# Kernel tuning notes

Hardware: AMD Instinct MI355X
Metric: run time of the kernel (lower is better)

Reference implementation:

```python
import jax, jax.numpy as jnp
import numpy as np

B, C, N = 8, 512, 2048  # batch, channels (=size), tokens


def setup_inputs() -> dict:
    key = jax.random.key(0)
    ks = jax.random.split(key, 9)
    s = 1.0 / np.sqrt(C)
    return {
        "q": jax.random.normal(ks[0], (B, C, N), dtype=jnp.float32),
        "k": jax.random.normal(ks[1], (B, C, N), dtype=jnp.float32),
        "v": jax.random.normal(ks[2], (B, C, N), dtype=jnp.float32),
        "wq": jax.random.normal(ks[3], (C, C), dtype=jnp.float32) * s,
        "bq": jax.random.normal(ks[4], (C,), dtype=jnp.float32) * s,
        "wk": jax.random.normal(ks[5], (C, C), dtype=jnp.float32) * s,
        "bk": jax.random.normal(ks[6], (C,), dtype=jnp.float32) * s,
        "wv": jax.random.normal(ks[7], (C, C), dtype=jnp.float32) * s,
        "bv": jax.random.normal(ks[8], (C,), dtype=jnp.float32) * s,
    }


def _proj(x, w, b):
    # 1x1 conv over channels: out[b,c,n] = sum_i w[c,i] x[b,i,n] + b[c]
    return jnp.einsum('ci,bin->bcn', w, x) + b[None, :, None]


def reference(q, k, v, wq, bq, wk, bk, wv, bv):
    residual = q                                   # [B, C, N]
    qp = _proj(q, wq, bq).transpose(0, 2, 1)       # [B, N, C]
    kp = _proj(k, wk, bk).transpose(0, 2, 1)       # [B, N, C]
    vp = _proj(v, wv, bv).transpose(0, 2, 1)       # [B, N, C]
    attn = jnp.einsum('bnc,bmc->bnm', qp, kp)      # raw QK^T, no scale/softmax
    out = jnp.einsum('bnm,bmc->bnc', attn, vp)     # [B, N, C]
    return out.transpose(0, 2, 1) + residual       # [B, C, N]
```

## Files before the change

### kernel.cpp

```cpp
#include <hip/hip_runtime.h>
#include <hip/hip_bf16.h>
#include <stdint.h>

#define B_ 8
#define C_ 512
#define N_ 2048

typedef __bf16 bf16_t;
typedef bf16_t bf16x8 __attribute__((ext_vector_type(8)));
typedef bf16_t bf16x4 __attribute__((ext_vector_type(4)));
typedef float f32x4 __attribute__((ext_vector_type(4)));

__global__ __launch_bounds__(256) void weights_kernel(
    const float* __restrict__ wq, const float* __restrict__ wk,
    const float* __restrict__ wv, const float* __restrict__ bq,
    const float* __restrict__ bk,
    bf16_t* __restrict__ WqT, bf16_t* __restrict__ WkT,
    bf16_t* __restrict__ Wvb, float* __restrict__ s1p)
{
    __shared__ bf16_t tile[64][65];
    __shared__ float red[256];
    const int t = blockIdx.x;
    const int tid = threadIdx.x;
    if (t < 128) {
        const float* src = (t < 64) ? wq : wk;
        bf16_t* dst = (t < 64) ? WqT : WkT;
        const int j = t & 63;
        const int i0 = (j & 7) * 64, c0 = (j >> 3) * 64;
        const int cx = (tid & 15) * 4, ry = tid >> 4;
#pragma unroll
        for (int r = ry; r < 64; r += 16) {
            float4 f = *(const float4*)&src[(size_t)(c0 + r) * C_ + i0 + cx];
            tile[r][cx + 0] = (bf16_t)f.x; tile[r][cx + 1] = (bf16_t)f.y;
            tile[r][cx + 2] = (bf16_t)f.z; tile[r][cx + 3] = (bf16_t)f.w;
        }
        __syncthreads();
#pragma unroll
        for (int r = ry; r < 64; r += 16) {
            bf16x4 o;
            o[0] = tile[cx + 0][r]; o[1] = tile[cx + 1][r];
            o[2] = tile[cx + 2][r]; o[3] = tile[cx + 3][r];
            *(bf16x4*)&dst[(size_t)(i0 + r) * C_ + c0 + cx] = o;
        }
    } else if (t < 192) {
        const int j = t - 128;
#pragma unroll
        for (int p = 0; p < 4; ++p) {
            const int i = j * 4096 + p * 1024 + tid * 4;
            float4 f = *(const float4*)(wv + i);
            bf16x4 o;
            o[0] = (bf16_t)f.x; o[1] = (bf16_t)f.y;
            o[2] = (bf16_t)f.z; o[3] = (bf16_t)f.w;
            *(bf16x4*)(Wvb + i) = o;
        }
    } else {
        float p = bk[tid] * bq[tid] + bk[tid + 256] * bq[tid + 256];
        red[tid] = p;
        __syncthreads();
        for (int s = 128; s > 0; s >>= 1) {
            if (tid < s) red[tid] += red[tid + s];
            __syncthreads();
        }
        if (tid == 0) s1p[0] = red[0];
    }
}

__global__ __launch_bounds__(256) void gemm_M_aux(
    const bf16_t* __restrict__ WqT, const bf16_t* __restrict__ WkT,
    bf16_t* __restrict__ M, const float* __restrict__ bq,
    const float* __restrict__ bk, float* __restrict__ gk,
    float* __restrict__ va)
{
    __shared__ __align__(16) bf16_t As[64 * 64];
    __shared__ __align__(16) bf16_t Bs[64 * 64];
    const int tid = threadIdx.x;
    if (blockIdx.x < 64) {
        const int lane = tid & 63, wave = tid >> 6;
        const int wr = wave >> 1, wc = wave & 1;
        const int m0 = (blockIdx.x >> 3) * 64, n0 = (blockIdx.x & 7) * 64;
        const int K = C_;
        f32x4 acc[2][2];
#pragma unroll
        for (int i = 0; i < 2; ++i)
#pragma unroll
            for (int j = 0; j < 2; ++j) acc[i][j] = 0.f;
        const int srow = tid >> 3;
        const int scol = ((tid & 7) ^ (srow & 7)) * 8;
        const int ldso = tid * 16;
        for (int t = 0; t < 8; ++t) {
            const bf16_t* ga = WqT + (size_t)(m0 + srow) * K + t * 64 + scol;
            const bf16_t* gb = WkT + (size_t)(n0 + srow) * K + t * 64 + scol;
#pragma unroll
            for (int p = 0; p < 2; ++p)
                __builtin_amdgcn_global_load_lds(
                    (const __attribute__((address_space(1))) void*)(ga + (size_t)p * 32 * K),
                    (__attribute__((address_space(3))) void*)((char*)As + ldso + p * 4096),
                    16, 0, 0);
#pragma unroll
            for (int p = 0; p < 2; ++p)
                __builtin_amdgcn_global_load_lds(
                    (const __attribute__((address_space(1))) void*)(gb + (size_t)p * 32 * K),
                    (__attribute__((address_space(3))) void*)((char*)Bs + ldso + p * 4096),
                    16, 0, 0);
            __syncthreads();
#pragma unroll
            for (int kk = 0; kk < 64; kk += 32) {
                bf16x8 af[2], bfr[2];
                const int kcol = kk + (lane >> 4) * 8;
                const int kc = kcol >> 3;
#pragma unroll
                for (int m = 0; m < 2; ++m) {
                    const int r = wr * 32 + (lane & 15) + m * 16;
                    af[m] = *(const bf16x8*)((const char*)As + r * 128 +
                                             ((kc ^ (r & 7)) << 4));
                }
#pragma unroll
                for (int n = 0; n < 2; ++n) {
                    const int r = wc * 32 + (lane & 15) + n * 16;
                    bfr[n] = *(const bf16x8*)((const char*)Bs + r * 128 +
                                              ((kc ^ (r & 7)) << 4));
                }
#pragma unroll
                for (int m = 0; m < 2; ++m)
#pragma unroll
                    for (int n = 0; n < 2; ++n)
                        acc[m][n] = __builtin_amdgcn_mfma_f32_16x16x32_bf16(
                            af[m], bfr[n], acc[m][n], 0, 0, 0);
            }
            __syncthreads();
        }
        const int rj = (lane >> 4) * 4;
        const int cc = lane & 15;
#pragma unroll
        for (int m = 0; m < 2; ++m)
#pragma unroll
            for (int n = 0; n < 2; ++n) {
                const int col = n0 + wc * 32 + n * 16 + cc;
                f32x4 vv = acc[m][n];
#pragma unroll
                for (int j = 0; j < 4; ++j) {
                    const int row = m0 + wr * 32 + m * 16 + rj + j;
                    M[(size_t)row * C_ + col] = (bf16_t)vv[j];
                }
            }
    } else {
        const int j = (int)blockIdx.x - 64;
        const bf16_t* W = (j < 8) ? WkT : WqT;
        const float* bb = (j < 8) ? bq : bk;
        float* out = (j < 8) ? gk : va;
        const int row = (j & 7) * 64 + (tid >> 2);
        const int c0 = (tid & 3) * 128;
        const bf16_t* rp = W + (size_t)row * C_ + c0;
        float acc = 0.f;
#pragma unroll
        for (int e = 0; e < 128; e += 8) {
            bf16x8 vv = *(const bf16x8*)(rp + e);
#pragma unroll
            for (int x = 0; x < 8; ++x) acc += (float)vv[x] * bb[c0 + e + x];
        }
        acc += __shfl_xor(acc, 1, 64);
        acc += __shfl_xor(acc, 2, 64);
        if ((tid & 3) == 0) out[row] = acc;
    }
}

__global__ __launch_bounds__(256) void prep_kernel(
    const float* __restrict__ kin, const float* __restrict__ vin,
    const float* __restrict__ q,
    bf16_t* __restrict__ kc, bf16_t* __restrict__ vc,
    bf16_t* __restrict__ qT, bf16_t* __restrict__ qc,
    float* __restrict__ sk, float* __restrict__ sv)
{
    __shared__ bf16_t tile[64][65];
    __shared__ float red[4];
    const int bid = blockIdx.x;
    const int tid = threadIdx.x;
    if (bid < 8192) {
        const int row = bid & 4095;
        const int selv = bid >> 12;
        const float* src = (selv ? vin : kin) + (size_t)row * N_;
        bf16_t* dst = (selv ? vc : kc) + (size_t)row * N_;
        const int i = tid * 8;
        float4 f0 = *(const float4*)(src + i);
        float4 f1 = *(const float4*)(src + i + 4);
        bf16x8 o;
        o[0] = (bf16_t)f0.x; o[1] = (bf16_t)f0.y; o[2] = (bf16_t)f0.z; o[3] = (bf16_t)f0.w;
        o[4] = (bf16_t)f1.x; o[5] = (bf16_t)f1.y; o[6] = (bf16_t)f1.z; o[7] = (bf16_t)f1.w;
        *(bf16x8*)(dst + i) = o;
        float s = f0.x + f0.y + f0.z + f0.w + f1.x + f1.y + f1.z + f1.w;
#pragma unroll
        for (int d = 1; d < 64; d <<= 1) s += __shfl_xor(s, d, 64);
        if ((tid & 63) == 0) red[tid >> 6] = s;
        __syncthreads();
        if (tid == 0)
            (selv ? sv : sk)[row] = red[0] + red[1] + red[2] + red[3];
    } else {
        const int t = bid - 8192;
        const int b = t >> 8;
        const int rem = t & 255;
        const int c0 = (rem >> 5) * 64;
        const int n0 = (rem & 31) * 64;
        const float* src = q + (size_t)b * C_ * N_;
        bf16_t* dT = qT + (size_t)b * N_ * C_;
        bf16_t* dc = qc + (size_t)b * C_ * N_;
        const int cx = (tid & 15) * 4, ry = tid >> 4;
#pragma unroll
        for (int r = ry; r < 64; r += 16) {
            float4 f = *(const float4*)&src[(size_t)(c0 + r) * N_ + n0 + cx];
            bf16x4 o;
            o[0] = (bf16_t)f.x; o[1] = (bf16_t)f.y;
            o[2] = (bf16_t)f.z; o[3] = (bf16_t)f.w;
            tile[r][cx + 0] = o[0]; tile[r][cx + 1] = o[1];
            tile[r][cx + 2] = o[2]; tile[r][cx + 3] = o[3];
            *(bf16x4*)&dc[(size_t)(c0 + r) * N_ + n0 + cx] = o;
        }
        __syncthreads();
#pragma unroll
        for (int r = ry; r < 64; r += 16) {
            bf16x4 o;
            o[0] = tile[cx + 0][r]; o[1] = tile[cx + 1][r];
            o[2] = tile[cx + 2][r]; o[3] = tile[cx + 3][r];
            *(bf16x4*)&dT[(size_t)(n0 + r) * C_ + c0 + cx] = o;
        }
    }
}

template <int SPLITS>
__global__ __launch_bounds__(256, 2) void gemm_ntK(
    const bf16_t* __restrict__ A, const bf16_t* __restrict__ Bm,
    bf16_t* __restrict__ Cout,
    int Nn, int K, size_t sA, size_t sB, size_t sC)
{
    __shared__ __align__(16) bf16_t As[128 * 64];
    __shared__ __align__(16) bf16_t Bs[128 * 64];

    const int tid = threadIdx.x, lane = tid & 63, wave = tid >> 6;
    const int wr = wave >> 1, wc = wave & 1;
    const int bz = blockIdx.z / SPLITS;
    const int sp = blockIdx.z % SPLITS;
    const int kbeg = sp * (K / SPLITS);
    const int nt = (K / SPLITS) / 64;

    const bf16_t* Ab = A + (size_t)bz * sA;
    const bf16_t* Bb = Bm + (size_t)bz * sB;
    const int m0 = blockIdx.y * 128, n0 = blockIdx.x * 128;

    f32x4 acc[4][4];
#pragma unroll
    for (int i = 0; i < 4; ++i)
#pragma unroll
        for (int j = 0; j < 4; ++j) acc[i][j] = 0.f;

    const int srow = tid >> 3;
    const int scol = ((tid & 7) ^ (srow & 7)) * 8;
    const int ldso = tid * 16;

    for (int t = 0; t < nt; ++t) {
        const bf16_t* ga = Ab + (size_t)(m0 + srow) * K + kbeg + t * 64 + scol;
        const bf16_t* gb = Bb + (size_t)(n0 + srow) * K + kbeg + t * 64 + scol;
#pragma unroll
        for (int p = 0; p < 4; ++p)
            __builtin_amdgcn_global_load_lds(
                (const __attribute__((address_space(1))) void*)(ga + (size_t)p * 32 * K),
                (__attribute__((address_space(3))) void*)((char*)As + ldso + p * 4096),
                16, 0, 0);
#pragma unroll
        for (int p = 0; p < 4; ++p)
            __builtin_amdgcn_global_load_lds(
                (const __attribute__((address_space(1))) void*)(gb + (size_t)p * 32 * K),
                (__attribute__((address_space(3))) void*)((char*)Bs + ldso + p * 4096),
                16, 0, 0);
        __syncthreads();

#pragma unroll
        for (int kk = 0; kk < 64; kk += 32) {
            bf16x8 af[4], bfr[4];
            const int kcol = kk + (lane >> 4) * 8;
            const int kc = kcol >> 3;
#pragma unroll
            for (int m = 0; m < 4; ++m) {
                const int r = wr * 64 + (lane & 15) + m * 16;
                af[m] = *(const bf16x8*)((const char*)As + r * 128 +
                                         ((kc ^ (r & 7)) << 4));
            }
#pragma unroll
            for (int n = 0; n < 4; ++n) {
                const int r = wc * 64 + (lane & 15) + n * 16;
                bfr[n] = *(const bf16x8*)((const char*)Bs + r * 128 +
                                          ((kc ^ (r & 7)) << 4));
            }
#pragma unroll
            for (int m = 0; m < 4; ++m)
#pragma unroll
                for (int n = 0; n < 4; ++n)
                    acc[m][n] = __builtin_amdgcn_mfma_f32_16x16x32_bf16(
                        af[m], bfr[n], acc[m][n], 0, 0, 0);
        }
        __syncthreads();
    }

    const int rj = (lane >> 4) * 4;
    const int cc = lane & 15;
#pragma unroll
    for (int m = 0; m < 4; ++m) {
#pragma unroll
        for (int n = 0; n < 4; ++n) {
            const int col = n0 + wc * 64 + n * 16 + cc;
            f32x4 vv = acc[m][n];
#pragma unroll
            for (int j = 0; j < 4; ++j) {
                const int row = m0 + wr * 64 + m * 16 + rj + j;
                Cout[(size_t)blockIdx.z * sC + (size_t)row * Nn + col] = (bf16_t)vv[j];
            }
        }
    }
}

__global__ __launch_bounds__(256) void reduce_mv_kernel(
    const bf16_t* __restrict__ Pt, bf16_t* __restrict__ Out,
    const bf16_t* __restrict__ Wvb, const bf16_t* __restrict__ M,
    const float* __restrict__ sk, const float* __restrict__ sv,
    const float* __restrict__ gk, const float* __restrict__ s1p,
    float* __restrict__ u, float* __restrict__ vbraw, float* __restrict__ s2)
{
    __shared__ float svec[C_];
    __shared__ float red[256];
    const size_t sCC = (size_t)C_ * C_;
    const int bid = blockIdx.x, tid = threadIdx.x;
    if (bid < 1024) {
        size_t idx = ((size_t)bid * 256 + tid) * 8;
        size_t b = idx / sCC;
        size_t r = idx - b * sCC;
        const bf16_t* base = Pt + (b * 4) * sCC + r;
        float acc[8];
#pragma unroll
        for (int j = 0; j < 8; ++j) acc[j] = 0.f;
#pragma unroll
        for (int s = 0; s < 4; ++s) {
            bf16x8 pv = *(const bf16x8*)(base + (size_t)s * sCC);
#pragma unroll
            for (int j = 0; j < 8; ++j) acc[j] += (float)pv[j];
        }
        bf16x8 o;
#pragma unroll
        for (int j = 0; j < 8; ++j) o[j] = (bf16_t)acc[j];
        *(bf16x8*)(Out + idx) = o;
    } else if (bid < 1032) {
        const int b = bid - 1024;
        const float* s4 = sv + (size_t)b * C_;
#pragma unroll
        for (int rr = 0; rr < 2; ++rr) {
            const int j = tid * 2 + rr;
            svec[j] = s4[j];
        }
        __syncthreads();
        const int c = tid * 2;
#pragma unroll
        for (int rr = 0; rr < 2; ++rr) {
            const bf16_t* row = Wvb + (size_t)(c + rr) * C_;
            float acc = 0.f;
            for (int j = 0; j < C_; j += 8) {
                bf16x8 vv = *(const bf16x8*)(row + j);
#pragma unroll
                for (int e = 0; e < 8; ++e) acc += (float)vv[e] * svec[j + e];
            }
            u[b * C_ + c + rr] = acc;
        }
    } else {
        const int b = bid - 1032;
        const float* s4 = sk + (size_t)b * C_;
#pragma unroll
        for (int rr = 0; rr < 2; ++rr) {
            const int j = tid * 2 + rr;
            svec[j] = s4[j];
        }
        __syncthreads();
        const int c = tid * 2;
#pragma unroll
        for (int rr = 0; rr < 2; ++rr) {
            const bf16_t* row = M + (size_t)(c + rr) * C_;
            float acc = 0.f;
            for (int j = 0; j < C_; j += 8) {
                bf16x8 vv = *(const bf16x8*)(row + j);
#pragma unroll
                for (int e = 0; e < 8; ++e) acc += (float)vv[e] * svec[j + e];
            }
            vbraw[b * C_ + c + rr] = acc;
        }
        float p = svec[tid] * gk[tid] + svec[tid + 256] * gk[tid + 256];
        red[tid] = p;
        __syncthreads();
        for (int s = 128; s > 0; s >>= 1) {
            if (tid < s) red[tid] += red[tid + s];
            __syncthreads();
        }
        if (tid == 0) s2[b] = red[0] + 2048.0f * s1p[0];
    }
}

template <int EPI>
__global__ __launch_bounds__(256) void gemm64_nt(
    const bf16_t* __restrict__ A, const bf16_t* __restrict__ Bm,
    bf16_t* __restrict__ Cout, size_t sA, size_t sB, size_t sC,
    const float* __restrict__ e0, const float* __restrict__ e1,
    const float* __restrict__ e2, const float* __restrict__ e3,
    const float* __restrict__ bqv, float* __restrict__ hout,
    const float* __restrict__ s1p, const float* __restrict__ s2p)
{
    __shared__ __align__(16) bf16_t As[64 * 64];
    __shared__ __align__(16) bf16_t Bs[64 * 64];

    const int tid = threadIdx.x, lane = tid & 63, wave = tid >> 6;
    const int wr = wave >> 1, wc = wave & 1;
    const int bz = blockIdx.z;
    const int m0 = blockIdx.y * 64, n0 = blockIdx.x * 64;
    const int K = C_;

    const bf16_t* Ab = A + (size_t)bz * sA;
    const bf16_t* Bb = Bm + (size_t)bz * sB;

    f32x4 acc[2][2];
#pragma unroll
    for (int i = 0; i < 2; ++i)
#pragma unroll
        for (int j = 0; j < 2; ++j) acc[i][j] = 0.f;

    const int srow = tid >> 3;
    const int scol = ((tid & 7) ^ (srow & 7)) * 8;
    const int ldso = tid * 16;

    float hacc = 0.f;
    const bool doH = (EPI == 3) && (blockIdx.x == 0);

    for (int t = 0; t < 8; ++t) {
        const bf16_t* ga = Ab + (size_t)(m0 + srow) * K + t * 64 + scol;
        const bf16_t* gb = Bb + (size_t)(n0 + srow) * K + t * 64 + scol;
#pragma unroll
        for (int p = 0; p < 2; ++p)
            __builtin_amdgcn_global_load_lds(
                (const __attribute__((address_space(1))) void*)(ga + (size_t)p * 32 * K),
                (__attribute__((address_space(3))) void*)((char*)As + ldso + p * 4096),
                16, 0, 0);
#pragma unroll
        for (int p = 0; p < 2; ++p)
            __builtin_amdgcn_global_load_lds(
                (const __attribute__((address_space(1))) void*)(gb + (size_t)p * 32 * K),
                (__attribute__((address_space(3))) void*)((char*)Bs + ldso + p * 4096),
                16, 0, 0);
        __syncthreads();

#pragma unroll
        for (int kk = 0; kk < 64; kk += 32) {
            bf16x8 af[2], bfr[2];
            const int kcol = kk + (lane >> 4) * 8;
            const int kc = kcol >> 3;
#pragma unroll
            for (int m = 0; m < 2; ++m) {
                const int r = wr * 32 + (lane & 15) + m * 16;
                af[m] = *(const bf16x8*)((const char*)As + r * 128 +
                                         ((kc ^ (r & 7)) << 4));
            }
#pragma unroll
            for (int n = 0; n < 2; ++n) {
                const int r = wc * 32 + (lane & 15) + n * 16;
                bfr[n] = *(const bf16x8*)((const char*)Bs + r * 128 +
                                          ((kc ^ (r & 7)) << 4));
            }
#pragma unroll
            for (int m = 0; m < 2; ++m)
#pragma unroll
                for (int n = 0; n < 2; ++n)
                    acc[m][n] = __builtin_amdgcn_mfma_f32_16x16x32_bf16(
                        af[m], bfr[n], acc[m][n], 0, 0, 0);
        }
        if (doH) {
            const int rr = tid >> 2, qq = tid & 3;
#pragma unroll
            for (int u = 0; u < 2; ++u) {
                const int c = qq * 2 + u;
                bf16x8 av = *(const bf16x8*)((const char*)As + rr * 128 +
                                             ((c ^ (rr & 7)) << 4));
                const float* bp = bqv + t * 64 + c * 8;
#pragma unroll
                for (int e = 0; e < 8; ++e) hacc += (float)av[e] * bp[e];
            }
        }
        __syncthreads();
    }

    const int rj = (lane >> 4) * 4;
    const int cc = lane & 15;
#pragma unroll
    for (int m = 0; m < 2; ++m) {
#pragma unroll
        for (int n = 0; n < 2; ++n) {
            const int col = n0 + wc * 32 + n * 16 + cc;
            f32x4 vv = acc[m][n];
#pragma unroll
            for (int j = 0; j < 4; ++j) {
                const int row = m0 + wr * 32 + m * 16 + rj + j;
                float val = vv[j];
                if (EPI == 3)
                    val += e0[bz * C_ + row] * e1[col] +
                           e2[row] * (e3[bz * C_ + col] + 2048.0f * e1[col]);
                Cout[(size_t)bz * sC + (size_t)row * C_ + col] = (bf16_t)val;
            }
        }
    }
    if (doH) {
        hacc += __shfl_xor(hacc, 1, 64);
        hacc += __shfl_xor(hacc, 2, 64);
        if ((tid & 3) == 0) {
            const int row = m0 + (tid >> 2);
            hout[bz * C_ + row] = hacc + e0[bz * C_ + row] * s1p[0] +
                                  e2[row] * s2p[bz];
        }
    }
}

__global__ __launch_bounds__(256) void gemm_final(
    const bf16_t* __restrict__ A, const bf16_t* __restrict__ Bm,
    float* __restrict__ Cout, const bf16_t* __restrict__ qc,
    const float* __restrict__ hvec)
{
    __shared__ __align__(16) bf16_t As[128 * 64];
    __shared__ __align__(16) bf16_t Bs[128 * 64];

    const int f = blockIdx.x;
    const int xcd = f & 7, sl = f >> 3;
    const int g = xcd + 8 * (sl >> 2);
    const int m0 = (sl & 3) * 128;
    const int bz = g >> 4;
    const int n0 = (g & 15) * 128;
    const int K = C_;

    const int tid = threadIdx.x, lane = tid & 63, wave = tid >> 6;
    const int wr = wave >> 1, wc = wave & 1;

    const bf16_t* Ab = A + (size_t)bz * ((size_t)C_ * C_);
    const bf16_t* Bb = Bm + (size_t)bz * ((size_t)N_ * C_);

    f32x4 acc[4][4];
#pragma unroll
    for (int i = 0; i < 4; ++i)
#pragma unroll
        for (int j = 0; j < 4; ++j) acc[i][j] = 0.f;

    const int srow = tid >> 3;
    const int scol = ((tid & 7) ^ (srow & 7)) * 8;
    const int ldso = tid * 16;

    for (int t = 0; t < 8; ++t) {
        const bf16_t* ga = Ab + (size_t)(m0 + srow) * K + t * 64 + scol;
        const bf16_t* gb = Bb + (size_t)(n0 + srow) * K + t * 64 + scol;
#pragma unroll
        for (int p = 0; p < 4; ++p)
            __builtin_amdgcn_global_load_lds(
                (const __attribute__((address_space(1))) void*)(ga + (size_t)p * 32 * K),
                (__attribute__((address_space(3))) void*)((char*)As + ldso + p * 4096),
                16, 0, 0);
#pragma unroll
        for (int p = 0; p < 4; ++p)
            __builtin_amdgcn_global_load_lds(
                (const __attribute__((address_space(1))) void*)(gb + (size_t)p * 32 * K),
                (__attribute__((address_space(3))) void*)((char*)Bs + ldso + p * 4096),
                16, 0, 0);
        __syncthreads();

#pragma unroll
        for (int kk = 0; kk < 64; kk += 32) {
            bf16x8 af[4], bfr[4];
            const int kcol = kk + (lane >> 4) * 8;
            const int kc = kcol >> 3;
#pragma unroll
            for (int m = 0; m < 4; ++m) {
                const int r = wr * 64 + (lane & 15) + m * 16;
                af[m] = *(const bf16x8*)((const char*)As + r * 128 +
                                         ((kc ^ (r & 7)) << 4));
            }
#pragma unroll
            for (int n = 0; n < 4; ++n) {
                const int r = wc * 64 + (lane & 15) + n * 16;
                bfr[n] = *(const bf16x8*)((const char*)Bs + r * 128 +
                                          ((kc ^ (r & 7)) << 4));
            }
#pragma unroll
            for (int m = 0; m < 4; ++m)
#pragma unroll
                for (int n = 0; n < 4; ++n)
                    acc[m][n] = __builtin_amdgcn_mfma_f32_16x16x32_bf16(
                        af[m], bfr[n], acc[m][n], 0, 0, 0);
        }
        __syncthreads();
    }

    const int rj = (lane >> 4) * 4;
    const int cc = lane & 15;
    const size_t ob = (size_t)bz * ((size_t)C_ * N_);
#pragma unroll
    for (int m = 0; m < 4; ++m) {
#pragma unroll
        for (int n = 0; n < 4; ++n) {
            const int col = n0 + wc * 64 + n * 16 + cc;
            f32x4 vv = acc[m][n];
#pragma unroll
            for (int j = 0; j < 4; ++j) {
                const int row = m0 + wr * 64 + m * 16 + rj + j;
                const size_t o = ob + (size_t)row * N_ + col;
                Cout[o] = vv[j] + hvec[bz * C_ + row] + (float)qc[o];
            }
        }
    }
}

extern "C" void kernel_launch(void* const* d_in, const int* in_sizes, int n_in,
                              void* d_out, int out_size, void* d_ws, size_t ws_size,
                              hipStream_t stream)
{
    (void)in_sizes; (void)n_in; (void)out_size; (void)ws_size;
    const float* q  = (const float*)d_in[0];
    const float* k  = (const float*)d_in[1];
    const float* v  = (const float*)d_in[2];
    const float* wq = (const float*)d_in[3];
    const float* bq = (const float*)d_in[4];
    const float* wk = (const float*)d_in[5];
    const float* bk = (const float*)d_in[6];
    const float* wv = (const float*)d_in[7];
    const float* bv = (const float*)d_in[8];
    float* out = (float*)d_out;

    char* ws = (char*)d_ws;
    const size_t WSZ = (size_t)C_ * C_ * 2;
    const size_t TSZ = (size_t)B_ * N_ * C_ * 2;
    const size_t SCZ = (size_t)B_ * C_ * C_ * 2;
    const size_t VSZ = (size_t)B_ * C_ * 4;
    const size_t sCC = (size_t)C_ * C_;
    const size_t sBN = (size_t)N_ * C_;
    size_t off = 0;
    bf16_t* WqTb = (bf16_t*)(ws + off); off += WSZ;
    bf16_t* WkTb = (bf16_t*)(ws + off); off += WSZ;
    bf16_t* Wvb  = (bf16_t*)(ws + off); off += WSZ;
    bf16_t* M    = (bf16_t*)(ws + off); off += WSZ;
    bf16_t* qT   = (bf16_t*)(ws + off); off += TSZ;
    bf16_t* qc   = (bf16_t*)(ws + off); off += TSZ;
    bf16_t* kc   = (bf16_t*)(ws + off); off += TSZ;
    bf16_t* vc   = (bf16_t*)(ws + off); off += TSZ;
    bf16_t* Dp   = (bf16_t*)(ws + off); off += TSZ;
    bf16_t* D    = (bf16_t*)(ws + off); off += SCZ;
    bf16_t* P1   = (bf16_t*)(ws + off); off += SCZ;
    bf16_t* HT   = (bf16_t*)(ws + off); off += SCZ;
    float*  sk   = (float*)(ws + off);  off += VSZ;
    float*  sv   = (float*)(ws + off);  off += VSZ;
    float*  gk   = (float*)(ws + off);  off += C_ * 4;
    float*  va   = (float*)(ws + off);  off += C_ * 4;
    float*  s1p  = (float*)(ws + off);  off += 64;
    float*  s2   = (float*)(ws + off);  off += 64;
    float*  uu   = (float*)(ws + off);  off += VSZ;
    float*  vbr  = (float*)(ws + off);  off += VSZ;
    float*  hb   = (float*)(ws + off);  off += VSZ;

    const dim3 blk(256);

    weights_kernel<<<dim3(193), blk, 0, stream>>>(
        wq, wk, wv, bq, bk, WqTb, WkTb, Wvb, s1p);

    gemm_M_aux<<<dim3(80), blk, 0, stream>>>(WqTb, WkTb, M, bq, bk, gk, va);

    prep_kernel<<<dim3(10240), blk, 0, stream>>>(
        k, v, q, kc, vc, qT, qc, sk, sv);

    gemm_ntK<4><<<dim3(C_ / 128, C_ / 128, B_ * 4), blk, 0, stream>>>(
        kc, vc, Dp, C_, N_, sBN, sBN, sCC);

    reduce_mv_kernel<<<dim3(1040), blk, 0, stream>>>(
        Dp, D, Wvb, M, sk, sv, gk, s1p, uu, vbr, s2);

    gemm64_nt<0><<<dim3(8, 8, B_), blk, 0, stream>>>(
        Wvb, D, P1, 0, sCC, sCC,
        nullptr, nullptr, nullptr, nullptr, nullptr, nullptr, nullptr, nullptr);

    gemm64_nt<3><<<dim3(8, 8, B_), blk, 0, stream>>>(
        P1, M, HT, sCC, 0, sCC, uu, va, bv, vbr, gk, hb, s1p, s2);

    gemm_final<<<dim3(512), blk, 0, stream>>>(HT, qT, out, qc, hb);
}
```

Before: 118.7 us.

## Fuse prep, weight and GEMM stages into fewer kernel launches

Merges the weight-conversion kernel into the input-prep kernel, moves the M=WqT·WkT GEMM and bias matvecs into the same launch as the split-K K·V^T GEMM, and fuses the split-K reduction with the Wv·D GEMM into one kernel. It also drops the bf16 copy of q and reads the fp32 residual directly in the final GEMM epilogue. The aim is to cut launch count from eight to five and remove one bf16 write/read pass over q, at the cost of heterogeneous blocks within each launch and a different residual precision path.

```diff
diff --git a/kernel.cpp b/kernel.cpp
--- a/kernel.cpp
+++ b/kernel.cpp
@@ -11,26 +11,33 @@
 typedef bf16_t bf16x4 __attribute__((ext_vector_type(4)));
 typedef float f32x4 __attribute__((ext_vector_type(4)));
 
-__global__ __launch_bounds__(256) void weights_kernel(
+__global__ __launch_bounds__(256) void prep_all_kernel(
+    const float* __restrict__ q, const float* __restrict__ kin,
+    const float* __restrict__ vin,
     const float* __restrict__ wq, const float* __restrict__ wk,
     const float* __restrict__ wv, const float* __restrict__ bq,
     const float* __restrict__ bk,
-    bf16_t* __restrict__ WqT, bf16_t* __restrict__ WkT,
-    bf16_t* __restrict__ Wvb, float* __restrict__ s1p)
+    bf16_t* __restrict__ qT, bf16_t* __restrict__ kc, bf16_t* __restrict__ vc,
+    bf16_t* __restrict__ WqT, bf16_t* __restrict__ WkT, bf16_t* __restrict__ Wvb,
+    float* __restrict__ s1p, float* __restrict__ sk, float* __restrict__ sv)
 {
     __shared__ bf16_t tile[64][65];
-    __shared__ float red[256];
-    const int t = blockIdx.x;
+    __shared__ float red256[256];
+    __shared__ float red4[4];
+    const int bid = blockIdx.x;
     const int tid = threadIdx.x;
-    if (t < 128) {
-        const float* src = (t < 64) ? wq : wk;
-        bf16_t* dst = (t < 64) ? WqT : WkT;
-        const int j = t & 63;
-        const int i0 = (j & 7) * 64, c0 = (j >> 3) * 64;
+
+    if (bid < 2048) {
+        const int b = bid >> 8;
+        const int rem = bid & 255;
+        const int c0 = (rem >> 5) * 64;
+        const int n0 = (rem & 31) * 64;
+        const float* src = q + (size_t)b * C_ * N_;
+        bf16_t* dT = qT + (size_t)b * N_ * C_;
         const int cx = (tid & 15) * 4, ry = tid >> 4;
 #pragma unroll
         for (int r = ry; r < 64; r += 16) {
-            float4 f = *(const float4*)&src[(size_t)(c0 + r) * C_ + i0 + cx];
+            float4 f = *(const float4*)&src[(size_t)(c0 + r) * N_ + n0 + cx];
             tile[r][cx + 0] = (bf16_t)f.x; tile[r][cx + 1] = (bf16_t)f.y;
             tile[r][cx + 2] = (bf16_t)f.z; tile[r][cx + 3] = (bf16_t)f.w;
         }
@@ -40,144 +47,55 @@
             bf16x4 o;
             o[0] = tile[cx + 0][r]; o[1] = tile[cx + 1][r];
             o[2] = tile[cx + 2][r]; o[3] = tile[cx + 3][r];
-            *(bf16x4*)&dst[(size_t)(i0 + r) * C_ + c0 + cx] = o;
-        }
-    } else if (t < 192) {
-        const int j = t - 128;
-#pragma unroll
-        for (int p = 0; p < 4; ++p) {
-            const int i = j * 4096 + p * 1024 + tid * 4;
-            float4 f = *(const float4*)(wv + i);
-            bf16x4 o;
-            o[0] = (bf16_t)f.x; o[1] = (bf16_t)f.y;
-            o[2] = (bf16_t)f.z; o[3] = (bf16_t)f.w;
-            *(bf16x4*)(Wvb + i) = o;
+            *(bf16x4*)&dT[(size_t)(n0 + r) * C_ + c0 + cx] = o;
+        }
+    } else if (bid < 2241) {
+        const int t = bid - 2048;
+        if (t < 128) {
+            const float* src = (t < 64) ? wq : wk;
+            bf16_t* dst = (t < 64) ? WqT : WkT;
+            const int j = t & 63;
+            const int i0 = (j & 7) * 64, c0 = (j >> 3) * 64;
+            const int cx = (tid & 15) * 4, ry = tid >> 4;
+#pragma unroll
+            for (int r = ry; r < 64; r += 16) {
+                float4 f = *(const float4*)&src[(size_t)(c0 + r) * C_ + i0 + cx];
+                tile[r][cx + 0] = (bf16_t)f.x; tile[r][cx + 1] = (bf16_t)f.y;
+                tile[r][cx + 2] = (bf16_t)f.z; tile[r][cx + 3] = (bf16_t)f.w;
+            }
+            __syncthreads();
+#pragma unroll
+            for (int r = ry; r < 64; r += 16) {
+                bf16x4 o;
+                o[0] = tile[cx + 0][r]; o[1] = tile[cx + 1][r];
+                o[2] = tile[cx + 2][r]; o[3] = tile[cx + 3][r];
+                *(bf16x4*)&dst[(size_t)(i0 + r) * C_ + c0 + cx] = o;
+            }
+        } else if (t < 192) {
+            const int j = t - 128;
+#pragma unroll
+            for (int p = 0; p < 4; ++p) {
+                const int i = j * 4096 + p * 1024 + tid * 4;
+                float4 f = *(const float4*)(wv + i);
+                bf16x4 o;
+                o[0] = (bf16_t)f.x; o[1] = (bf16_t)f.y;
+                o[2] = (bf16_t)f.z; o[3] = (bf16_t)f.w;
+                *(bf16x4*)(Wvb + i) = o;
+            }
+        } else {
+            float p = bk[tid] * bq[tid] + bk[tid + 256] * bq[tid + 256];
+            red256[tid] = p;
+            __syncthreads();
+            for (int s = 128; s > 0; s >>= 1) {
+                if (tid < s) red256[tid] += red256[tid + s];
+                __syncthreads();
+            }
+            if (tid == 0) s1p[0] = red256[0];
         }
     } else {
-        float p = bk[tid] * bq[tid] + bk[tid + 256] * bq[tid + 256];
-        red[tid] = p;
-        __syncthreads();
-        for (int s = 128; s > 0; s >>= 1) {
-            if (tid < s) red[tid] += red[tid + s];
-            __syncthreads();
-        }
-        if (tid == 0) s1p[0] = red[0];
-    }
-}
-
-__global__ __launch_bounds__(256) void gemm_M_aux(
-    const bf16_t* __restrict__ WqT, const bf16_t* __restrict__ WkT,
-    bf16_t* __restrict__ M, const float* __restrict__ bq,
-    const float* __restrict__ bk, float* __restrict__ gk,
-    float* __restrict__ va)
-{
-    __shared__ __align__(16) bf16_t As[64 * 64];
-    __shared__ __align__(16) bf16_t Bs[64 * 64];
-    const int tid = threadIdx.x;
-    if (blockIdx.x < 64) {
-        const int lane = tid & 63, wave = tid >> 6;
-        const int wr = wave >> 1, wc = wave & 1;
-        const int m0 = (blockIdx.x >> 3) * 64, n0 = (blockIdx.x & 7) * 64;
-        const int K = C_;
-        f32x4 acc[2][2];
-#pragma unroll
-        for (int i = 0; i < 2; ++i)
-#pragma unroll
-            for (int j = 0; j < 2; ++j) acc[i][j] = 0.f;
-        const int srow = tid >> 3;
-        const int scol = ((tid & 7) ^ (srow & 7)) * 8;
-        const int ldso = tid * 16;
-        for (int t = 0; t < 8; ++t) {
-            const bf16_t* ga = WqT + (size_t)(m0 + srow) * K + t * 64 + scol;
-            const bf16_t* gb = WkT + (size_t)(n0 + srow) * K + t * 64 + scol;
-#pragma unroll
-            for (int p = 0; p < 2; ++p)
-                __builtin_amdgcn_global_load_lds(
-                    (const __attribute__((address_space(1))) void*)(ga + (size_t)p * 32 * K),
-                    (__attribute__((address_space(3))) void*)((char*)As + ldso + p * 4096),
-                    16, 0, 0);
-#pragma unroll
-            for (int p = 0; p < 2; ++p)
-                __builtin_amdgcn_global_load_lds(
-                    (const __attribute__((address_space(1))) void*)(gb + (size_t)p * 32 * K),
-                    (__attribute__((address_space(3))) void*)((char*)Bs + ldso + p * 4096),
-                    16, 0, 0);
-            __syncthreads();
-#pragma unroll
-            for (int kk = 0; kk < 64; kk += 32) {
-                bf16x8 af[2], bfr[2];
-                const int kcol = kk + (lane >> 4) * 8;
-                const int kc = kcol >> 3;
-#pragma unroll
-                for (int m = 0; m < 2; ++m) {
-                    const int r = wr * 32 + (lane & 15) + m * 16;
-                    af[m] = *(const bf16x8*)((const char*)As + r * 128 +
-                                             ((kc ^ (r & 7)) << 4));
-                }
-#pragma unroll
-                for (int n = 0; n < 2; ++n) {
-                    const int r = wc * 32 + (lane & 15) + n * 16;
-                    bfr[n] = *(const bf16x8*)((const char*)Bs + r * 128 +
-                                              ((kc ^ (r & 7)) << 4));
-                }
-#pragma unroll
-                for (int m = 0; m < 2; ++m)
-#pragma unroll
-                    for (int n = 0; n < 2; ++n)
-                        acc[m][n] = __builtin_amdgcn_mfma_f32_16x16x32_bf16(
-                            af[m], bfr[n], acc[m][n], 0, 0, 0);
-            }
-            __syncthreads();
-        }
-        const int rj = (lane >> 4) * 4;
-        const int cc = lane & 15;
-#pragma unroll
-        for (int m = 0; m < 2; ++m)
-#pragma unroll
-            for (int n = 0; n < 2; ++n) {
-                const int col = n0 + wc * 32 + n * 16 + cc;
-                f32x4 vv = acc[m][n];
-#pragma unroll
-                for (int j = 0; j < 4; ++j) {
-                    const int row = m0 + wr * 32 + m * 16 + rj + j;
-                    M[(size_t)row * C_ + col] = (bf16_t)vv[j];
-                }
-            }
-    } else {
-        const int j = (int)blockIdx.x - 64;
-        const bf16_t* W = (j < 8) ? WkT : WqT;
-        const float* bb = (j < 8) ? bq : bk;
-        float* out = (j < 8) ? gk : va;
-        const int row = (j & 7) * 64 + (tid >> 2);
-        const int c0 = (tid & 3) * 128;
-        const bf16_t* rp = W + (size_t)row * C_ + c0;
-        float acc = 0.f;
-#pragma unroll
-        for (int e = 0; e < 128; e += 8) {
-            bf16x8 vv = *(const bf16x8*)(rp + e);
-#pragma unroll
-            for (int x = 0; x < 8; ++x) acc += (float)vv[x] * bb[c0 + e + x];
-        }
-        acc += __shfl_xor(acc, 1, 64);
-        acc += __shfl_xor(acc, 2, 64);
-        if ((tid & 3) == 0) out[row] = acc;
-    }
-}
-
-__global__ __launch_bounds__(256) void prep_kernel(
-    const float* __restrict__ kin, const float* __restrict__ vin,
-    const float* __restrict__ q,
-    bf16_t* __restrict__ kc, bf16_t* __restrict__ vc,
-    bf16_t* __restrict__ qT, bf16_t* __restrict__ qc,
-    float* __restrict__ sk, float* __restrict__ sv)
-{
-    __shared__ bf16_t tile[64][65];
-    __shared__ float red[4];
-    const int bid = blockIdx.x;
-    const int tid = threadIdx.x;
-    if (bid < 8192) {
-        const int row = bid & 4095;
-        const int selv = bid >> 12;
+        const int r = bid - 2241;
+        const int row = r & 4095;
+        const int selv = r >> 12;
         const float* src = (selv ? vin : kin) + (size_t)row * N_;
         bf16_t* dst = (selv ? vc : kc) + (size_t)row * N_;
         const int i = tid * 8;
@@ -190,169 +108,286 @@
         float s = f0.x + f0.y + f0.z + f0.w + f1.x + f1.y + f1.z + f1.w;
 #pragma unroll
         for (int d = 1; d < 64; d <<= 1) s += __shfl_xor(s, d, 64);
-        if ((tid & 63) == 0) red[tid >> 6] = s;
+        if ((tid & 63) == 0) red4[tid >> 6] = s;
         __syncthreads();
         if (tid == 0)
-            (selv ? sv : sk)[row] = red[0] + red[1] + red[2] + red[3];
-    } else {
-        const int t = bid - 8192;
-        const int b = t >> 8;
-        const int rem = t & 255;
-        const int c0 = (rem >> 5) * 64;
-        const int n0 = (rem & 31) * 64;
-        const float* src = q + (size_t)b * C_ * N_;
-        bf16_t* dT = qT + (size_t)b * N_ * C_;
-        bf16_t* dc = qc + (size_t)b * C_ * N_;
-        const int cx = (tid & 15) * 4, ry = tid >> 4;
-#pragma unroll
-        for (int r = ry; r < 64; r += 16) {
-            float4 f = *(const float4*)&src[(size_t)(c0 + r) * N_ + n0 + cx];
-            bf16x4 o;
-            o[0] = (bf16_t)f.x; o[1] = (bf16_t)f.y;
-            o[2] = (bf16_t)f.z; o[3] = (bf16_t)f.w;
-            tile[r][cx + 0] = o[0]; tile[r][cx + 1] = o[1];
-            tile[r][cx + 2] = o[2]; tile[r][cx + 3] = o[3];
-            *(bf16x4*)&dc[(size_t)(c0 + r) * N_ + n0 + cx] = o;
-        }
-        __syncthreads();
-#pragma unroll
-        for (int r = ry; r < 64; r += 16) {
-            bf16x4 o;
-            o[0] = tile[cx + 0][r]; o[1] = tile[cx + 1][r];
-            o[2] = tile[cx + 2][r]; o[3] = tile[cx + 3][r];
-            *(bf16x4*)&dT[(size_t)(n0 + r) * C_ + c0 + cx] = o;
-        }
+            (selv ? sv : sk)[row] = red4[0] + red4[1] + red4[2] + red4[3];
     }
 }
 
-template <int SPLITS>
-__global__ __launch_bounds__(256, 2) void gemm_ntK(
-    const bf16_t* __restrict__ A, const bf16_t* __restrict__ Bm,
-    bf16_t* __restrict__ Cout,
-    int Nn, int K, size_t sA, size_t sB, size_t sC)
+__global__ __launch_bounds__(256, 2) void dkv_M_kernel(
+    const bf16_t* __restrict__ kc, const bf16_t* __restrict__ vc,
+    bf16_t* __restrict__ Dp,
+    const bf16_t* __restrict__ WqT, const bf16_t* __restrict__ WkT,
+    bf16_t* __restrict__ M, const float* __restrict__ bq,
+    const float* __restrict__ bk, float* __restrict__ gk,
+    float* __restrict__ va)
 {
     __shared__ __align__(16) bf16_t As[128 * 64];
     __shared__ __align__(16) bf16_t Bs[128 * 64];
-
+    const int f = blockIdx.x;
     const int tid = threadIdx.x, lane = tid & 63, wave = tid >> 6;
     const int wr = wave >> 1, wc = wave & 1;
-    const int bz = blockIdx.z / SPLITS;
-    const int sp = blockIdx.z % SPLITS;
-    const int kbeg = sp * (K / SPLITS);
-    const int nt = (K / SPLITS) / 64;
-
-    const bf16_t* Ab = A + (size_t)bz * sA;
-    const bf16_t* Bb = Bm + (size_t)bz * sB;
-    const int m0 = blockIdx.y * 128, n0 = blockIdx.x * 128;
-
-    f32x4 acc[4][4];
-#pragma unroll
-    for (int i = 0; i < 4; ++i)
-#pragma unroll
-        for (int j = 0; j < 4; ++j) acc[i][j] = 0.f;
-
-    const int srow = tid >> 3;
-    const int scol = ((tid & 7) ^ (srow & 7)) * 8;
-    const int ldso = tid * 16;
-
-    for (int t = 0; t < nt; ++t) {
-        const bf16_t* ga = Ab + (size_t)(m0 + srow) * K + kbeg + t * 64 + scol;
-        const bf16_t* gb = Bb + (size_t)(n0 + srow) * K + kbeg + t * 64 + scol;
-#pragma unroll
-        for (int p = 0; p < 4; ++p)
-            __builtin_amdgcn_global_load_lds(
-                (const __attribute__((address_space(1))) void*)(ga + (size_t)p * 32 * K),
-                (__attribute__((address_space(3))) void*)((char*)As + ldso + p * 4096),
-                16, 0, 0);
-#pragma unroll
-        for (int p = 0; p < 4; ++p)
-            __builtin_amdgcn_global_load_lds(
-                (const __attribute__((address_space(1))) void*)(gb + (size_t)p * 32 * K),
-                (__attribute__((address_space(3))) void*)((char*)Bs + ldso + p * 4096),
-                16, 0, 0);
-        __syncthreads();
-
-#pragma unroll
-        for (int kk = 0; kk < 64; kk += 32) {
-            bf16x8 af[4], bfr[4];
-            const int kcol = kk + (lane >> 4) * 8;
-            const int kc = kcol >> 3;
-#pragma unroll
-            for (int m = 0; m < 4; ++m) {
-                const int r = wr * 64 + (lane & 15) + m * 16;
-                af[m] = *(const bf16x8*)((const char*)As + r * 128 +
-                                         ((kc ^ (r & 7)) << 4));
-            }
+    const size_t sCC = (size_t)C_ * C_;
+    const size_t sBN = (size_t)N_ * C_;
+
+    if (f < 512) {
+        const int zz = f >> 4;
+        const int bz = zz >> 2, sp = zz & 3;
+        const int t4 = f & 15;
+        const int m0 = (t4 >> 2) * 128, n0 = (t4 & 3) * 128;
+        const int kbeg = sp * 512;
+        const bf16_t* Ab = kc + (size_t)bz * sBN;
+        const bf16_t* Bb = vc + (size_t)bz * sBN;
+
+        f32x4 acc[4][4];
+#pragma unroll
+        for (int i = 0; i < 4; ++i)
+#pragma unroll
+            for (int j = 0; j < 4; ++j) acc[i][j] = 0.f;
+
+        const int srow = tid >> 3;
+        const int scol = ((tid & 7) ^ (srow & 7)) * 8;
+        const int ldso = tid * 16;
+
+        for (int t = 0; t < 8; ++t) {
+            const bf16_t* ga = Ab + (size_t)(m0 + srow) * N_ + kbeg + t * 64 + scol;
+            const bf16_t* gb = Bb + (size_t)(n0 + srow) * N_ + kbeg + t * 64 + scol;
+#pragma unroll
+            for (int p = 0; p < 4; ++p)
+                __builtin_amdgcn_global_load_lds(
+                    (const __attribute__((address_space(1))) void*)(ga + (size_t)p * 32 * N_),
+                    (__attribute__((address_space(3))) void*)((char*)As + ldso + p * 4096),
+                    16, 0, 0);
+#pragma unroll
+            for (int p = 0; p < 4; ++p)
+                __builtin_amdgcn_global_load_lds(
+                    (const __attribute__((address_space(1))) void*)(gb + (size_t)p * 32 * N_),
+                    (__attribute__((address_space(3))) void*)((char*)Bs + ldso + p * 4096),
+                    16, 0, 0);
+            __syncthreads();
+
+#pragma unroll
+            for (int kk = 0; kk < 64; kk += 32) {
+                bf16x8 af[4], bfr[4];
+                const int kcol = kk + (lane >> 4) * 8;
+                const int kcn = kcol >> 3;
+#pragma unroll
+                for (int m = 0; m < 4; ++m) {
+                    const int r = wr * 64 + (lane & 15) + m * 16;
+                    af[m] = *(const bf16x8*)((const char*)As + r * 128 +
+                                             ((kcn ^ (r & 7)) << 4));
+                }
+#pragma unroll
+                for (int n = 0; n < 4; ++n) {
+                    const int r = wc * 64 + (lane & 15) + n * 16;
+                    bfr[n] = *(const bf16x8*)((const char*)Bs + r * 128 +
+                                              ((kcn ^ (r & 7)) << 4));
+                }
+#pragma unroll
+                for (int m = 0; m < 4; ++m)
+#pragma unroll
+                    for (int n = 0; n < 4; ++n)
+                        acc[m][n] = __builtin_amdgcn_mfma_f32_16x16x32_bf16(
+                            af[m], bfr[n], acc[m][n], 0, 0, 0);
+            }
+            __syncthreads();
+        }
+
+        const int rj = (lane >> 4) * 4;
+        const int cc = lane & 15;
+#pragma unroll
+        for (int m = 0; m < 4; ++m)
 #pragma unroll
             for (int n = 0; n < 4; ++n) {
-                const int r = wc * 64 + (lane & 15) + n * 16;
-                bfr[n] = *(const bf16x8*)((const char*)Bs + r * 128 +
-                                          ((kc ^ (r & 7)) << 4));
-            }
-#pragma unroll
-            for (int m = 0; m < 4; ++m)
-#pragma unroll
-                for (int n = 0; n < 4; ++n)
-                    acc[m][n] = __builtin_amdgcn_mfma_f32_16x16x32_bf16(
-                        af[m], bfr[n], acc[m][n], 0, 0, 0);
-        }
-        __syncthreads();
-    }
-
-    const int rj = (lane >> 4) * 4;
-    const int cc = lane & 15;
-#pragma unroll
-    for (int m = 0; m < 4; ++m) {
-#pragma unroll
-        for (int n = 0; n < 4; ++n) {
-            const int col = n0 + wc * 64 + n * 16 + cc;
-            f32x4 vv = acc[m][n];
-#pragma unroll
-            for (int j = 0; j < 4; ++j) {
-                const int row = m0 + wr * 64 + m * 16 + rj + j;
-                Cout[(size_t)blockIdx.z * sC + (size_t)row * Nn + col] = (bf16_t)vv[j];
-            }
-        }
+                const int col = n0 + wc * 64 + n * 16 + cc;
+                f32x4 vv = acc[m][n];
+#pragma unroll
+                for (int j = 0; j < 4; ++j) {
+                    const int row = m0 + wr * 64 + m * 16 + rj + j;
+                    Dp[(size_t)zz * sCC + (size_t)row * C_ + col] = (bf16_t)vv[j];
+                }
+            }
+    } else if (f < 576) {
+        const int g = f - 512;
+        const int m0 = (g >> 3) * 64, n0 = (g & 7) * 64;
+        f32x4 acc[2][2];
+#pragma unroll
+        for (int i = 0; i < 2; ++i)
+#pragma unroll
+            for (int j = 0; j < 2; ++j) acc[i][j] = 0.f;
+        const int srow = tid >> 3;
+        const int scol = ((tid & 7) ^ (srow & 7)) * 8;
+        const int ldso = tid * 16;
+        for (int t = 0; t < 8; ++t) {
+            const bf16_t* ga = WqT + (size_t)(m0 + srow) * C_ + t * 64 + scol;
+            const bf16_t* gb = WkT + (size_t)(n0 + srow) * C_ + t * 64 + scol;
+#pragma unroll
+            for (int p = 0; p < 2; ++p)
+                __builtin_amdgcn_global_load_lds(
+                    (const __attribute__((address_space(1))) void*)(ga + (size_t)p * 32 * C_),
+                    (__attribute__((address_space(3))) void*)((char*)As + ldso + p * 4096),
+                    16, 0, 0);
+#pragma unroll
+            for (int p = 0; p < 2; ++p)
+                __builtin_amdgcn_global_load_lds(
+                    (const __attribute__((address_space(1))) void*)(gb + (size_t)p * 32 * C_),
+                    (__attribute__((address_space(3))) void*)((char*)Bs + ldso + p * 4096),
+                    16, 0, 0);
+            __syncthreads();
+#pragma unroll
+            for (int kk = 0; kk < 64; kk += 32) {
+                bf16x8 af[2], bfr[2];
+                const int kcol = kk + (lane >> 4) * 8;
+                const int kcn = kcol >> 3;
+#pragma unroll
+                for (int m = 0; m < 2; ++m) {
+                    const int r = wr * 32 + (lane & 15) + m * 16;
+                    af[m] = *(const bf16x8*)((const char*)As + r * 128 +
+                                             ((kcn ^ (r & 7)) << 4));
+                }
+#pragma unroll
+                for (int n = 0; n < 2; ++n) {
+                    const int r = wc * 32 + (lane & 15) + n * 16;
+                    bfr[n] = *(const bf16x8*)((const char*)Bs + r * 128 +
+                                              ((kcn ^ (r & 7)) << 4));
+                }
+#pragma unroll
+                for (int m = 0; m < 2; ++m)
+#pragma unroll
+                    for (int n = 0; n < 2; ++n)
+                        acc[m][n] = __builtin_amdgcn_mfma_f32_16x16x32_bf16(
+                            af[m], bfr[n], acc[m][n], 0, 0, 0);
+            }
+            __syncthreads();
+        }
+        const int rj = (lane >> 4) * 4;
+        const int cc = lane & 15;
+#pragma unroll
+        for (int m = 0; m < 2; ++m)
+#pragma unroll
+            for (int n = 0; n < 2; ++n) {
+                const int col = n0 + wc * 32 + n * 16 + cc;
+                f32x4 vv = acc[m][n];
+#pragma unroll
+                for (int j = 0; j < 4; ++j) {
+                    const int row = m0 + wr * 32 + m * 16 + rj + j;
+                    M[(size_t)row * C_ + col] = (bf16_t)vv[j];
+                }
+            }
+    } else {
+        const int j = f - 576;
+        const bf16_t* W = (j < 8) ? WkT : WqT;
+        const float* bb = (j < 8) ? bq : bk;
+        float* out = (j < 8) ? gk : va;
+        const int row = (j & 7) * 64 + (tid >> 2);
+        const int c0 = (tid & 3) * 128;
+        const bf16_t* rp = W + (size_t)row * C_ + c0;
+        float acc = 0.f;
+#pragma unroll
+        for (int e = 0; e < 128; e += 8) {
+            bf16x8 vv = *(const bf16x8*)(rp + e);
+#pragma unroll
+            for (int x = 0; x < 8; ++x) acc += (float)vv[x] * bb[c0 + e + x];
+        }
+        acc += __shfl_xor(acc, 1, 64);
+        acc += __shfl_xor(acc, 2, 64);
+        if ((tid & 3) == 0) out[row] = acc;
     }
 }
 
-__global__ __launch_bounds__(256) void reduce_mv_kernel(
-    const bf16_t* __restrict__ Pt, bf16_t* __restrict__ Out,
-    const bf16_t* __restrict__ Wvb, const bf16_t* __restrict__ M,
+__global__ __launch_bounds__(256) void p1_fused_kernel(
+    const bf16_t* __restrict__ Wvb, const bf16_t* __restrict__ Dp,
+    bf16_t* __restrict__ P1, const bf16_t* __restrict__ M,
     const float* __restrict__ sk, const float* __restrict__ sv,
     const float* __restrict__ gk, const float* __restrict__ s1p,
     float* __restrict__ u, float* __restrict__ vbraw, float* __restrict__ s2)
 {
+    __shared__ __align__(16) bf16_t As[64 * 64];
+    __shared__ __align__(16) bf16_t Bs[64 * 64];
     __shared__ float svec[C_];
     __shared__ float red[256];
+    const int f = blockIdx.x;
+    const int tid = threadIdx.x, lane = tid & 63, wave = tid >> 6;
+    const int wr = wave >> 1, wc = wave & 1;
     const size_t sCC = (size_t)C_ * C_;
-    const int bid = blockIdx.x, tid = threadIdx.x;
-    if (bid < 1024) {
-        size_t idx = ((size_t)bid * 256 + tid) * 8;
-        size_t b = idx / sCC;
-        size_t r = idx - b * sCC;
-        const bf16_t* base = Pt + (b * 4) * sCC + r;
-        float acc[8];
-#pragma unroll
-        for (int j = 0; j < 8; ++j) acc[j] = 0.f;
-#pragma unroll
-        for (int s = 0; s < 4; ++s) {
-            bf16x8 pv = *(const bf16x8*)(base + (size_t)s * sCC);
-#pragma unroll
-            for (int j = 0; j < 8; ++j) acc[j] += (float)pv[j];
-        }
-        bf16x8 o;
-#pragma unroll
-        for (int j = 0; j < 8; ++j) o[j] = (bf16_t)acc[j];
-        *(bf16x8*)(Out + idx) = o;
-    } else if (bid < 1032) {
-        const int b = bid - 1024;
+
+    if (f < 512) {
+        const int bz = f >> 6;
+        const int m0 = ((f >> 3) & 7) * 64, n0 = (f & 7) * 64;
+        f32x4 acc[2][2];
+#pragma unroll
+        for (int i = 0; i < 2; ++i)
+#pragma unroll
+            for (int j = 0; j < 2; ++j) acc[i][j] = 0.f;
+        const int srow = tid >> 3;
+        const int scol = ((tid & 7) ^ (srow & 7)) * 8;
+        const int ldso = tid * 16;
+
+        for (int sp = 0; sp < 4; ++sp) {
+            const bf16_t* Bb = Dp + (size_t)(bz * 4 + sp) * sCC;
+            for (int t = 0; t < 8; ++t) {
+                const bf16_t* ga = Wvb + (size_t)(m0 + srow) * C_ + t * 64 + scol;
+                const bf16_t* gb = Bb + (size_t)(n0 + srow) * C_ + t * 64 + scol;
+#pragma unroll
+                for (int p = 0; p < 2; ++p)
+                    __builtin_amdgcn_global_load_lds(
+                        (const __attribute__((address_space(1))) void*)(ga + (size_t)p * 32 * C_),
+                        (__attribute__((address_space(3))) void*)((char*)As + ldso + p * 4096),
+                        16, 0, 0);
+#pragma unroll
+                for (int p = 0; p < 2; ++p)
+                    __builtin_amdgcn_global_load_lds(
+                        (const __attribute__((address_space(1))) void*)(gb + (size_t)p * 32 * C_),
+                        (__attribute__((address_space(3))) void*)((char*)Bs + ldso + p * 4096),
+                        16, 0, 0);
+                __syncthreads();
+#pragma unroll
+                for (int kk = 0; kk < 64; kk += 32) {
+                    bf16x8 af[2], bfr[2];
+                    const int kcol = kk + (lane >> 4) * 8;
+                    const int kcn = kcol >> 3;
+#pragma unroll
+                    for (int m = 0; m < 2; ++m) {
+                        const int r = wr * 32 + (lane & 15) + m * 16;
+                        af[m] = *(const bf16x8*)((const char*)As + r * 128 +
+                                                 ((kcn ^ (r & 7)) << 4));
+                    }
+#pragma unroll
+                    for (int n = 0; n < 2; ++n) {
+                        const int r = wc * 32 + (lane & 15) + n * 16;
+                        bfr[n] = *(const bf16x8*)((const char*)Bs + r * 128 +
+                                                  ((kcn ^ (r & 7)) << 4));
+                    }
+#pragma unroll
+                    for (int m = 0; m < 2; ++m)
+#pragma unroll
+                        for (int n = 0; n < 2; ++n)
+                            acc[m][n] = __builtin_amdgcn_mfma_f32_16x16x32_bf16(
+                                af[m], bfr[n], acc[m][n], 0, 0, 0);
+                }
+                __syncthreads();
+            }
+        }
+        const int rj = (lane >> 4) * 4;
+        const int cc = lane & 15;
+#pragma unroll
+        for (int m = 0; m < 2; ++m)
+#pragma unroll
+            for (int n = 0; n < 2; ++n) {
+                const int col = n0 + wc * 32 + n * 16 + cc;
+                f32x4 vv = acc[m][n];
+#pragma unroll
+                for (int j = 0; j < 4; ++j) {
+                    const int row = m0 + wr * 32 + m * 16 + rj + j;
+                    P1[(size_t)bz * sCC + (size_t)row * C_ + col] = (bf16_t)vv[j];
+                }
+            }
+    } else if (f < 520) {
+        const int b = f - 512;
         const float* s4 = sv + (size_t)b * C_;
-#pragma unroll
-        for (int rr = 0; rr < 2; ++rr) {
-            const int j = tid * 2 + rr;
-            svec[j] = s4[j];
-        }
+        svec[tid * 2] = s4[tid * 2];
+        svec[tid * 2 + 1] = s4[tid * 2 + 1];
         __syncthreads();
         const int c = tid * 2;
 #pragma unroll
@@ -367,13 +402,10 @@
             u[b * C_ + c + rr] = acc;
         }
     } else {
-        const int b = bid - 1032;
+        const int b = f - 520;
         const float* s4 = sk + (size_t)b * C_;
-#pragma unroll
-        for (int rr = 0; rr < 2; ++rr) {
-            const int j = tid * 2 + rr;
-            svec[j] = s4[j];
-        }
+        svec[tid * 2] = s4[tid * 2];
+        svec[tid * 2 + 1] = s4[tid * 2 + 1];
         __syncthreads();
         const int c = tid * 2;
 #pragma unroll
@@ -398,10 +430,9 @@
     }
 }
 
-template <int EPI>
-__global__ __launch_bounds__(256) void gemm64_nt(
+__global__ __launch_bounds__(256) void gemm_ht(
     const bf16_t* __restrict__ A, const bf16_t* __restrict__ Bm,
-    bf16_t* __restrict__ Cout, size_t sA, size_t sB, size_t sC,
+    bf16_t* __restrict__ Cout,
     const float* __restrict__ e0, const float* __restrict__ e1,
     const float* __restrict__ e2, const float* __restrict__ e3,
     const float* __restrict__ bqv, float* __restrict__ hout,
@@ -414,10 +445,9 @@
     const int wr = wave >> 1, wc = wave & 1;
     const int bz = blockIdx.z;
     const int m0 = blockIdx.y * 64, n0 = blockIdx.x * 64;
-    const int K = C_;
-
-    const bf16_t* Ab = A + (size_t)bz * sA;
-    const bf16_t* Bb = Bm + (size_t)bz * sB;
+    const size_t sCC = (size_t)C_ * C_;
+
+    const bf16_t* Ab = A + (size_t)bz * sCC;
 
     f32x4 acc[2][2];
 #pragma unroll
@@ -430,21 +460,21 @@
     const int ldso = tid * 16;
 
     float hacc = 0.f;
-    const bool doH = (EPI == 3) && (blockIdx.x == 0);
+    const bool doH = (blockIdx.x == 0);
 
     for (int t = 0; t < 8; ++t) {
-        const bf16_t* ga = Ab + (size_t)(m0 + srow) * K + t * 64 + scol;
-        const bf16_t* gb = Bb + (size_t)(n0 + srow) * K + t * 64 + scol;
+        const bf16_t* ga = Ab + (size_t)(m0 + srow) * C_ + t * 64 + scol;
+        const bf16_t* gb = Bm + (size_t)(n0 + srow) * C_ + t * 64 + scol;
 #pragma unroll
         for (int p = 0; p < 2; ++p)
             __builtin_amdgcn_global_load_lds(
-                (const __attribute__((address_space(1))) void*)(ga + (size_t)p * 32 * K),
+                (const __attribute__((address_space(1))) void*)(ga + (size_t)p * 32 * C_),
                 (__attribute__((address_space(3))) void*)((char*)As + ldso + p * 4096),
                 16, 0, 0);
 #pragma unroll
         for (int p = 0; p < 2; ++p)
             __builtin_amdgcn_global_load_lds(
-                (const __attribute__((address_space(1))) void*)(gb + (size_t)p * 32 * K),
+                (const __attribute__((address_space(1))) void*)(gb + (size_t)p * 32 * C_),
                 (__attribute__((address_space(3))) void*)((char*)Bs + ldso + p * 4096),
                 16, 0, 0);
         __syncthreads();
@@ -453,18 +483,18 @@
         for (int kk = 0; kk < 64; kk += 32) {
             bf16x8 af[2], bfr[2];
             const int kcol = kk + (lane >> 4) * 8;
-            const int kc = kcol >> 3;
+            const int kcn = kcol >> 3;
 #pragma unroll
             for (int m = 0; m < 2; ++m) {
                 const int r = wr * 32 + (lane & 15) + m * 16;
                 af[m] = *(const bf16x8*)((const char*)As + r * 128 +
-                                         ((kc ^ (r & 7)) << 4));
+                                         ((kcn ^ (r & 7)) << 4));
             }
 #pragma unroll
             for (int n = 0; n < 2; ++n) {
                 const int r = wc * 32 + (lane & 15) + n * 16;
                 bfr[n] = *(const bf16x8*)((const char*)Bs + r * 128 +
-                                          ((kc ^ (r & 7)) << 4));
+                                          ((kcn ^ (r & 7)) << 4));
             }
 #pragma unroll
             for (int m = 0; m < 2; ++m)
@@ -476,8 +506,8 @@
         if (doH) {
             const int rr = tid >> 2, qq = tid & 3;
 #pragma unroll
-            for (int u = 0; u < 2; ++u) {
-                const int c = qq * 2 + u;
+            for (int uq = 0; uq < 2; ++uq) {
+                const int c = qq * 2 + uq;
                 bf16x8 av = *(const bf16x8*)((const char*)As + rr * 128 +
                                              ((c ^ (rr & 7)) << 4));
                 const float* bp = bqv + t * 64 + c * 8;
@@ -499,11 +529,9 @@
 #pragma unroll
             for (int j = 0; j < 4; ++j) {
                 const int row = m0 + wr * 32 + m * 16 + rj + j;
-                float val = vv[j];
-                if (EPI == 3)
-                    val += e0[bz * C_ + row] * e1[col] +
-                           e2[row] * (e3[bz * C_ + col] + 2048.0f * e1[col]);
-                Cout[(size_t)bz * sC + (size_t)row * C_ + col] = (bf16_t)val;
+                float val = vv[j] + e0[bz * C_ + row] * e1[col] +
+                            e2[row] * (e3[bz * C_ + col] + 2048.0f * e1[col]);
+                Cout[(size_t)bz * sCC + (size_t)row * C_ + col] = (bf16_t)val;
             }
         }
     }
@@ -520,7 +548,7 @@
 
 __global__ __launch_bounds__(256) void gemm_final(
     const bf16_t* __restrict__ A, const bf16_t* __restrict__ Bm,
-    float* __restrict__ Cout, const bf16_t* __restrict__ qc,
+    float* __restrict__ Cout, const float* __restrict__ qres,
     const float* __restrict__ hvec)
 {
     __shared__ __align__(16) bf16_t As[128 * 64];
@@ -571,18 +599,18 @@
         for (int kk = 0; kk < 64; kk += 32) {
             bf16x8 af[4], bfr[4];
             const int kcol = kk + (lane >> 4) * 8;
-            const int kc = kcol >> 3;
+            const int kcn = kcol >> 3;
 #pragma unroll
             for (int m = 0; m < 4; ++m) {
                 const int r = wr * 64 + (lane & 15) + m * 16;
                 af[m] = *(const bf16x8*)((const char*)As + r * 128 +
-                                         ((kc ^ (r & 7)) << 4));
+                                         ((kcn ^ (r & 7)) << 4));
             }
 #pragma unroll
             for (int n = 0; n < 4; ++n) {
                 const int r = wc * 64 + (lane & 15) + n * 16;
                 bfr[n] = *(const bf16x8*)((const char*)Bs + r * 128 +
-                                          ((kc ^ (r & 7)) << 4));
+                                          ((kcn ^ (r & 7)) << 4));
             }
 #pragma unroll
             for (int m = 0; m < 4; ++m)
@@ -607,7 +635,7 @@
             for (int j = 0; j < 4; ++j) {
                 const int row = m0 + wr * 64 + m * 16 + rj + j;
                 const size_t o = ob + (size_t)row * N_ + col;
-                Cout[o] = vv[j] + hvec[bz * C_ + row] + (float)qc[o];
+                Cout[o] = vv[j] + hvec[bz * C_ + row] + qres[o];
             }
         }
     }
@@ -635,18 +663,15 @@
     const size_t SCZ = (size_t)B_ * C_ * C_ * 2;
     const size_t VSZ = (size_t)B_ * C_ * 4;
     const size_t sCC = (size_t)C_ * C_;
-    const size_t sBN = (size_t)N_ * C_;
     size_t off = 0;
     bf16_t* WqTb = (bf16_t*)(ws + off); off += WSZ;
     bf16_t* WkTb = (bf16_t*)(ws + off); off += WSZ;
     bf16_t* Wvb  = (bf16_t*)(ws + off); off += WSZ;
     bf16_t* M    = (bf16_t*)(ws + off); off += WSZ;
     bf16_t* qT   = (bf16_t*)(ws + off); off += TSZ;
-    bf16_t* qc   = (bf16_t*)(ws + off); off += TSZ;
     bf16_t* kc   = (bf16_t*)(ws + off); off += TSZ;
     bf16_t* vc   = (bf16_t*)(ws + off); off += TSZ;
     bf16_t* Dp   = (bf16_t*)(ws + off); off += TSZ;
-    bf16_t* D    = (bf16_t*)(ws + off); off += SCZ;
     bf16_t* P1   = (bf16_t*)(ws + off); off += SCZ;
     bf16_t* HT   = (bf16_t*)(ws + off); off += SCZ;
     float*  sk   = (float*)(ws + off);  off += VSZ;
@@ -661,26 +686,17 @@
 
     const dim3 blk(256);
 
-    weights_kernel<<<dim3(193), blk, 0, stream>>>(
-        wq, wk, wv, bq, bk, WqTb, WkTb, Wvb, s1p);
-
-    gemm_M_aux<<<dim3(80), blk, 0, stream>>>(WqTb, WkTb, M, bq, bk, gk, va);
-
-    prep_kernel<<<dim3(10240), blk, 0, stream>>>(
-        k, v, q, kc, vc, qT, qc, sk, sv);
-
-    gemm_ntK<4><<<dim3(C_ / 128, C_ / 128, B_ * 4), blk, 0, stream>>>(
-        kc, vc, Dp, C_, N_, sBN, sBN, sCC);
-
-    reduce_mv_kernel<<<dim3(1040), blk, 0, stream>>>(
-        Dp, D, Wvb, M, sk, sv, gk, s1p, uu, vbr, s2);
-
-    gemm64_nt<0><<<dim3(8, 8, B_), blk, 0, stream>>>(
-        Wvb, D, P1, 0, sCC, sCC,
-        nullptr, nullptr, nullptr, nullptr, nullptr, nullptr, nullptr, nullptr);
-
-    gemm64_nt<3><<<dim3(8, 8, B_), blk, 0, stream>>>(
-        P1, M, HT, sCC, 0, sCC, uu, va, bv, vbr, gk, hb, s1p, s2);
-
-    gemm_final<<<dim3(512), blk, 0, stream>>>(HT, qT, out, qc, hb);
+    prep_all_kernel<<<dim3(10433), blk, 0, stream>>>(
+        q, k, v, wq, wk, wv, bq, bk, qT, kc, vc, WqTb, WkTb, Wvb, s1p, sk, sv);
+
+    dkv_M_kernel<<<dim3(592), blk, 0, stream>>>(
+        kc, vc, Dp, WqTb, WkTb, M, bq, bk, gk, va);
+
+    p1_fused_kernel<<<dim3(528), blk, 0, stream>>>(
+        Wvb, Dp, P1, M, sk, sv, gk, s1p, uu, vbr, s2);
+
+    gemm_ht<<<dim3(8, 8, B_), blk, 0, stream>>>(
+        P1, M, HT, uu, va, bv, vbr, gk, hb, s1p, s2);
+
+    gemm_final<<<dim3(512), blk, 0, stream>>>(HT, qT, out, q, hb);
 }
```

New measurement: 111.2 us. 6.3% less time.
